# Optimization experiments

Measured on AMD Instinct MI355X. Metric: run time of the kernel, lower is better.

## Reference

```python
import jax, jax.numpy as jnp
import numpy as np

N_HEAD = 16


def setup_inputs() -> dict:
    key = jax.random.key(0)
    k1, k2, k3 = jax.random.split(key, 3)
    B, T, C = 2, 2048, 1024
    x = jax.random.normal(k1, (B, T, C), dtype=jnp.float32)
    # Linear params (torch Linear: y = x @ W.T + b), scaled for stability
    w_attn = jax.random.normal(k2, (3 * C, C), dtype=jnp.float32) * (C ** -0.5)
    b_attn = jnp.zeros((3 * C,), dtype=jnp.float32)
    w_proj = jax.random.normal(k3, (C, C), dtype=jnp.float32) * (C ** -0.5)
    b_proj = jnp.zeros((C,), dtype=jnp.float32)
    return {"x": x, "w_attn": w_attn, "b_attn": b_attn,
            "w_proj": w_proj, "b_proj": b_proj}


def reference(x, w_attn, b_attn, w_proj, b_proj):
    B, T, C = x.shape
    H = N_HEAD
    hd = C // H
    # qkv projection: [B, T, 3C]
    qkv = jnp.einsum('btc,dc->btd', x, w_attn) + b_attn
    # NOTE: original views as (B, T, H, 3*hd) then splits last dim -> per-head
    # interleaved qkv layout (NOT the standard 3-way split of full projection).
    qkv = qkv.reshape(B, T, H, 3 * hd).transpose(0, 2, 1, 3)  # [B, H, T, 3*hd]
    q, k, v = qkv[..., :hd], qkv[..., hd:2 * hd], qkv[..., 2 * hd:]
    # NOTE: scale uses full embedding dim C, not head_dim (faithful to source).
    attn = jnp.einsum('bhqd,bhkd->bhqk', q, k) * (C ** -0.5)
    # NOTE: no causal mask in the original despite the class name.
    attn = jax.nn.softmax(attn, axis=-1)
    y = jnp.einsum('bhqk,bhkd->bhqd', attn, v)  # [B, H, T, hd]
    y = y.transpose(0, 2, 1, 3).reshape(B, T, C)
    y = jnp.einsum('btc,dc->btd', y, w_proj) + b_proj
    return y
```

## Files before the change

kernel.cpp:

```cpp
#include <hip/hip_runtime.h>
#include <hip/hip_bf16.h>

typedef unsigned short u16;
typedef __bf16 bf16x8 __attribute__((ext_vector_type(8)));
typedef float f32x4 __attribute__((ext_vector_type(4)));
typedef float f32x16 __attribute__((ext_vector_type(16)));
typedef unsigned u32x4 __attribute__((ext_vector_type(4)));

#define QSCALE 0.045084220027780106f

__device__ __forceinline__ u16 f2b(float f) {
  unsigned x = __float_as_uint(f);
  unsigned r = (x + 0x7fffu + ((x >> 16) & 1u)) >> 16;
  return (u16)r;
}

__device__ __forceinline__ void gll16(const void* g, void* l) {
  __builtin_amdgcn_global_load_lds((const __attribute__((address_space(1))) void*)g,
                                   (__attribute__((address_space(3))) void*)l, 16, 0, 0);
}

__device__ __forceinline__ f32x4 mfma16(bf16x8 a, bf16x8 b, f32x4 c) {
  return __builtin_amdgcn_mfma_f32_16x16x32_bf16(a, b, c, 0, 0, 0);
}
__device__ __forceinline__ f32x16 mfma32(bf16x8 a, bf16x8 b, f32x16 c) {
  return __builtin_amdgcn_mfma_f32_32x32x16_bf16(a, b, c, 0, 0, 0);
}

__device__ __forceinline__ void plswap(unsigned& a, unsigned& b) {
  asm volatile("v_permlane32_swap_b32 %0, %1" : "+v"(a), "+v"(b));
}
__device__ __forceinline__ unsigned cvtpk(float lo, float hi) {
  unsigned r;
  asm("v_cvt_pk_bf16_f32 %0, %1, %2" : "=v"(r) : "v"(lo), "v"(hi));
  return r;
}

#if __has_builtin(__builtin_amdgcn_exp2f)
__device__ __forceinline__ float fexp2(float x) { return __builtin_amdgcn_exp2f(x); }
#else
__device__ __forceinline__ float fexp2(float x) {
  float r;
  asm("v_exp_f32 %0, %1" : "=v"(r) : "v"(x));
  return r;
}
#endif

#define WAITV(N) asm volatile("s_waitcnt vmcnt(" #N ")" ::: "memory")
#define BAR()                              \
  do {                                     \
    __builtin_amdgcn_s_barrier();          \
    __builtin_amdgcn_sched_barrier(0);     \
  } while (0)

__global__ __launch_bounds__(256) void cvt3(const float* __restrict__ x,
                                            const float* __restrict__ wa,
                                            const float* __restrict__ wp,
                                            u16* __restrict__ dx,
                                            u16* __restrict__ dwa,
                                            u16* __restrict__ dwp) {
  const int N1 = 4194304, N2 = 3145728;
  int i = (blockIdx.x * 256 + threadIdx.x) * 4;
  const float* s;
  u16* d;
  int off;
  if (i < N1) { s = x; d = dx; off = i; }
  else if (i < N1 + N2) { s = wa; d = dwa; off = i - N1; }
  else { s = wp; d = dwp; off = i - N1 - N2; }
  float4 v = *(const float4*)(s + off);
  ushort4 o;
  o.x = f2b(v.x); o.y = f2b(v.y); o.z = f2b(v.z); o.w = f2b(v.w);
  *(ushort4*)(d + off) = o;
}

__global__ __launch_bounds__(256) void gemm_qkv(const u16* __restrict__ A,
                                                const u16* __restrict__ W,
                                                const float* __restrict__ bias,
                                                u16* __restrict__ Qb,
                                                u16* __restrict__ Kb,
                                                u16* __restrict__ Vtb) {
  __shared__ u16 As[2][128 * 64];
  __shared__ u16 Bs[2][192 * 64];
  const int K = 1024;
  int o = blockIdx.x;
  int xcd = o & 7, li = o >> 3;
  int bm = (xcd >> 1) * 8 + (li >> 3);
  int bn = (xcd & 1) * 8 + (li & 7);
  int tid = threadIdx.x, lane = tid & 63, w = tid >> 6;
  int wm = w >> 1, wn = w & 1, g = lane >> 4, c = lane & 15;
  f32x4 acc[4][6] = {};
  const u16* Arow = A + (size_t)(bm * 128) * K;
  const u16* Wrow = W + (size_t)(bn * 192) * K;

  const u16* asrc[4];
  const u16* bsrc[6];
  int adst[4], bdst[6];
#pragma unroll
  for (int rr = 0; rr < 4; ++rr) {
    int ci = rr * 256 + tid;
    int row = ci >> 3, sseg = (ci & 7) ^ (row & 7);
    asrc[rr] = Arow + (size_t)row * K + sseg * 8;
    adst[rr] = ci * 8;
  }
#pragma unroll
  for (int rr = 0; rr < 6; ++rr) {
    int ci = rr * 256 + tid;
    int row = ci >> 3, sseg = (ci & 7) ^ (row & 7);
    bsrc[rr] = Wrow + (size_t)row * K + sseg * 8;
    bdst[rr] = ci * 8;
  }
  auto stage = [&](int buf) {
#pragma unroll
    for (int rr = 0; rr < 4; ++rr) gll16(asrc[rr], &As[buf][adst[rr]]);
#pragma unroll
    for (int rr = 0; rr < 6; ++rr) gll16(bsrc[rr], &Bs[buf][bdst[rr]]);
#pragma unroll
    for (int rr = 0; rr < 4; ++rr) asrc[rr] += 64;
#pragma unroll
    for (int rr = 0; rr < 6; ++rr) bsrc[rr] += 64;
  };

  stage(0);
  for (int t = 0; t < 16; ++t) {
    int cur = t & 1;
    if (t < 15) {
      stage(cur ^ 1);
      WAITV(10);
    } else {
      WAITV(0);
    }
    BAR();
#pragma unroll
    for (int kk = 0; kk < 2; ++kk) {
      int q = kk * 4 + g;
      bf16x8 af[4], bfr[6];
#pragma unroll
      for (int mi = 0; mi < 4; ++mi) {
        int row = wm * 64 + mi * 16 + c;
        af[mi] = *(const bf16x8*)&As[cur][row * 64 + ((q ^ (row & 7)) * 8)];
      }
#pragma unroll
      for (int ni = 0; ni < 6; ++ni) {
        int row = wn * 96 + ni * 16 + c;
        bfr[ni] = *(const bf16x8*)&Bs[cur][row * 64 + ((q ^ (row & 7)) * 8)];
      }
      __builtin_amdgcn_s_setprio(1);
#pragma unroll
      for (int mi = 0; mi < 4; ++mi)
#pragma unroll
        for (int ni = 0; ni < 6; ++ni)
          acc[mi][ni] = mfma16(af[mi], bfr[ni], acc[mi][ni]);
      __builtin_amdgcn_s_setprio(0);
    }
    BAR();
  }

  __syncthreads();
  u16* VT = &As[0][0];
  int b = bm >> 4;
  int tbase = (bm & 15) << 7;
  int bh = b * 16 + bn;

  int cls[6], qkoff[6], vb[6], vx[6];
  float bi[6];
#pragma unroll
  for (int ni = 0; ni < 6; ++ni) {
    int j = wn * 96 + ni * 16 + c;
    bi[ni] = bias[bn * 192 + j];
    if (j < 64) { cls[ni] = 0; qkoff[ni] = bh * 131072 + j; }
    else if (j < 128) { cls[ni] = 1; qkoff[ni] = bh * 131072 + (j - 64); }
    else { cls[ni] = 2; int vcl = j - 128; vb[ni] = vcl * 128; vx[ni] = (vcl & 15) << 3; }
  }
#pragma unroll
  for (int mi = 0; mi < 4; ++mi)
#pragma unroll
    for (int r = 0; r < 4; ++r) {
      int trow = wm * 64 + mi * 16 + g * 4 + r;
      int t = tbase + trow;
#pragma unroll
      for (int ni = 0; ni < 6; ++ni) {
        float v = acc[mi][ni][r] + bi[ni];
        if (cls[ni] == 0) Qb[(size_t)qkoff[ni] + t * 64] = f2b(v * QSCALE);
        else if (cls[ni] == 1) Kb[(size_t)qkoff[ni] + t * 64] = f2b(v);
        else VT[vb[ni] + (trow ^ vx[ni])] = f2b(v);
      }
    }
  __syncthreads();
  for (int id = tid; id < 64 * 16; id += 256) {
    int vcl = id >> 4, tc = id & 15;
    bf16x8 vv = *(const bf16x8*)&VT[vcl * 128 + ((tc * 8) ^ ((vcl & 15) << 3))];
    size_t dst = ((size_t)bh * 64 + vcl) * 2048 + tbase + tc * 8;
    *(bf16x8*)&Vtb[dst] = vv;
  }
}

__global__ __launch_bounds__(256, 4) void attn_kernel(const u16* __restrict__ Qb,
                                                      const u16* __restrict__ Kb,
                                                      const u16* __restrict__ Vtb,
                                                      u16* __restrict__ Yb) {
  __shared__ u16 SMEM[2][2][2][2048];
  int bh = blockIdx.y;
  int b = bh >> 4, hh = bh & 15;
  int tid = threadIdx.x, lane = tid & 63, wv = tid >> 6;
  int wq = wv & 1, wk = wv >> 1;
  int c5 = lane & 31, h = lane >> 5;
  int q0 = blockIdx.x * 64 + wq * 32;
  const u16* Qh = Qb + (size_t)bh * 2048 * 64;
  const u16* Kh = Kb + (size_t)bh * 2048 * 64;
  const u16* Vh = Vtb + (size_t)bh * 64 * 2048;

  const u16* Qrow = Qh + (size_t)(q0 + c5) * 64;
  bf16x8 qf[4];
#pragma unroll
  for (int dc = 0; dc < 4; ++dc)
    qf[dc] = *(const bf16x8*)&Qrow[dc * 16 + h * 8];

  f32x16 acc0 = {}, acc1 = {};
  float ls = 0.f;

  const u16* gsrc[4];
  int gstep[4];
  u16* ld0[4];
  u16* ld1[4];
#pragma unroll
  for (int part = 0; part < 4; ++part) {
    int ci = part * 256 + tid;
    int st = ci >> 9;
    int rem = ci & 511;
    int kv = rem >> 8;
    int slot = rem & 255;
    int row = slot >> 3, seg = slot & 7;
    int sseg = seg ^ (row & 7);
    int t0 = st * 1024;
    if (kv == 0) {
      gsrc[part] = Kh + (size_t)(t0 + row) * 64 + sseg * 8;
      gstep[part] = 32 * 64;
    } else {
      int dh = sseg >> 2, ksl = sseg & 3;
      gsrc[part] = Vh + (size_t)(dh * 32 + row) * 2048 + t0 + ksl * 8;
      gstep[part] = 32;
    }
    ld0[part] = &SMEM[st][0][kv][slot * 8];
    ld1[part] = &SMEM[st][1][kv][slot * 8];
  }
  auto stagepair = [&](int buf) {
#pragma unroll
    for (int part = 0; part < 4; ++part) {
      gll16(gsrc[part], buf ? ld1[part] : ld0[part]);
      gsrc[part] += gstep[part];
    }
  };

  auto tilecompute = [&](int cur) {
    const u16* Kt = &SMEM[wk][cur][0][0];
    const u16* Vt = &SMEM[wk][cur][1][0];

    f32x16 s0 = {};
    __builtin_amdgcn_s_setprio(1);
#pragma unroll
    for (int dc = 0; dc < 4; ++dc) {
      bf16x8 kf = *(const bf16x8*)&Kt[c5 * 64 + (((dc * 2 + h) ^ (c5 & 7)) * 8)];
      s0 = mfma32(kf, qf[dc], s0);
    }
    __builtin_amdgcn_s_setprio(0);

#pragma unroll
    for (int j = 0; j < 16; ++j) s0[j] = fexp2(s0[j]);
    float t4[4];
#pragma unroll
    for (int i = 0; i < 4; ++i)
      t4[i] = (s0[i] + s0[i + 4]) + (s0[i + 8] + s0[i + 12]);
    ls += (t4[0] + t4[1]) + (t4[2] + t4[3]);

    unsigned w0[8];
#pragma unroll
    for (int q2 = 0; q2 < 4; ++q2)
#pragma unroll
      for (int pp = 0; pp < 2; ++pp)
        w0[q2 * 2 + pp] = cvtpk(s0[q2 * 4 + 2 * pp], s0[q2 * 4 + 2 * pp + 1]);

    __builtin_amdgcn_s_setprio(1);
#pragma unroll
    for (int ks2 = 0; ks2 < 2; ++ks2) {
      unsigned a0 = w0[4 * ks2 + 0], b0 = w0[4 * ks2 + 2];
      unsigned a1 = w0[4 * ks2 + 1], b1 = w0[4 * ks2 + 3];
      plswap(a0, b0);
      plswap(a1, b1);
      u32x4 aw = {a0, a1, b0, b1};
      bf16x8 af = __builtin_bit_cast(bf16x8, aw);
      bf16x8 vf0 = *(const bf16x8*)&Vt[c5 * 64 + (((ks2 * 2 + h) ^ (c5 & 7)) * 8)];
      bf16x8 vf1 = *(const bf16x8*)&Vt[c5 * 64 + (((4 + ks2 * 2 + h) ^ (c5 & 7)) * 8)];
      acc0 = mfma32(af, vf0, acc0);
      acc1 = mfma32(af, vf1, acc1);
    }
    __builtin_amdgcn_s_setprio(0);
  };

  stagepair(0);
  for (int it2 = 0; it2 < 16; ++it2) {
    stagepair(1);
    WAITV(4);
    BAR();
    tilecompute(0);
    BAR();
    if (it2 < 15) {
      stagepair(0);
      WAITV(4);
    } else {
      WAITV(0);
    }
    BAR();
    tilecompute(1);
    BAR();
  }

  float* MG = (float*)&SMEM[0][0][0][0];
  int gi = wq * 64 + lane;
  __syncthreads();
  if (wk == 1) {
    MG[gi] = ls;
#pragma unroll
    for (int j = 0; j < 16; ++j) {
      MG[128 + gi * 33 + j] = acc0[j];
      MG[128 + gi * 33 + 16 + j] = acc1[j];
    }
  }
  __syncthreads();
  if (wk == 0) {
    float l2 = ls + MG[gi];
    l2 += __shfl_xor(l2, 32);
    float inv = 1.0f / l2;
#pragma unroll
    for (int j = 0; j < 16; ++j) {
      int q = (j & 3) + 8 * (j >> 2) + 4 * h;
      float ibq = __shfl(inv, q, 64);
      float y0 = (acc0[j] + MG[128 + gi * 33 + j]) * ibq;
      float y1 = (acc1[j] + MG[128 + gi * 33 + 16 + j]) * ibq;
      int trow = q0 + q;
      size_t base = ((size_t)b * 2048 + trow) * 1024 + hh * 64;
      Yb[base + c5] = f2b(y0);
      Yb[base + 32 + c5] = f2b(y1);
    }
  }
}

__global__ __launch_bounds__(512) void gemm_proj(const u16* __restrict__ A,
                                                 const u16* __restrict__ W,
                                                 const float* __restrict__ bias,
                                                 float* __restrict__ out) {
  __shared__ u16 As[4][128 * 64];
  __shared__ u16 Bs[4][128 * 64];
  const int K = 1024;
  int o = blockIdx.x;
  int bn = o & 7, bm = o >> 3;
  int tid = threadIdx.x, lane = tid & 63, w = tid >> 6;
  int wm = w >> 1, wn = w & 1, g = lane >> 4, c = lane & 15;
  f32x4 acc[2][4] = {};
  const u16* Arow = A + (size_t)(bm * 128) * K;
  const u16* Wrow = W + (size_t)(bn * 128) * K;

  const u16* asrc[2];
  const u16* bsrc[2];
  int sdst[2];
#pragma unroll
  for (int rr = 0; rr < 2; ++rr) {
    int ci = rr * 512 + tid;
    int row = ci >> 3, sseg = (ci & 7) ^ (row & 7);
    asrc[rr] = Arow + (size_t)row * K + sseg * 8;
    bsrc[rr] = Wrow + (size_t)row * K + sseg * 8;
    sdst[rr] = ci * 8;
  }
  auto stage = [&](int step) {
    int slot = step & 3;
#pragma unroll
    for (int rr = 0; rr < 2; ++rr) gll16(asrc[rr], &As[slot][sdst[rr]]);
#pragma unroll
    for (int rr = 0; rr < 2; ++rr) gll16(bsrc[rr], &Bs[slot][sdst[rr]]);
#pragma unroll
    for (int rr = 0; rr < 2; ++rr) { asrc[rr] += 64; bsrc[rr] += 64; }
  };

  auto compute = [&](int step) {
    int slot = step & 3;
#pragma unroll
    for (int kk = 0; kk < 2; ++kk) {
      int q = kk * 4 + g;
      bf16x8 af[2], bfr[4];
#pragma unroll
      for (int mi = 0; mi < 2; ++mi) {
        int row = wm * 32 + mi * 16 + c;
        af[mi] = *(const bf16x8*)&As[slot][row * 64 + ((q ^ (row & 7)) * 8)];
      }
#pragma unroll
      for (int ni = 0; ni < 4; ++ni) {
        int row = wn * 64 + ni * 16 + c;
        bfr[ni] = *(const bf16x8*)&Bs[slot][row * 64 + ((q ^ (row & 7)) * 8)];
      }
#pragma unroll
      for (int mi = 0; mi < 2; ++mi)
#pragma unroll
        for (int ni = 0; ni < 4; ++ni)
          acc[mi][ni] = mfma16(af[mi], bfr[ni], acc[mi][ni]);
    }
  };

  stage(0);
  stage(1);
  stage(2);
  for (int t = 0; t <= 13; ++t) {
    WAITV(8);
    BAR();
    if (t <= 12) stage(t + 3);
    compute(t);
  }
  WAITV(4);
  BAR();
  compute(14);
  WAITV(0);
  BAR();
  compute(15);

#pragma unroll
  for (int mi = 0; mi < 2; ++mi)
#pragma unroll
    for (int ni = 0; ni < 4; ++ni)
#pragma unroll
      for (int r = 0; r < 4; ++r) {
        int row = bm * 128 + wm * 32 + mi * 16 + g * 4 + r;
        int col = bn * 128 + wn * 64 + ni * 16 + c;
        out[(size_t)row * 1024 + col] = acc[mi][ni][r] + bias[col];
      }
}

extern "C" void kernel_launch(void* const* d_in, const int* in_sizes, int n_in,
                              void* d_out, int out_size, void* d_ws, size_t ws_size,
                              hipStream_t stream) {
  const float* x      = (const float*)d_in[0];
  const float* w_attn = (const float*)d_in[1];
  const float* b_attn = (const float*)d_in[2];
  const float* w_proj = (const float*)d_in[3];
  const float* b_proj = (const float*)d_in[4];
  float* out = (float*)d_out;

  u16* ws = (u16*)d_ws;
  const size_t XB  = 0;
  const size_t WAB = XB + 4194304;
  const size_t WPB = WAB + 3145728;
  const size_t QB  = WPB + 1048576;
  const size_t KB  = QB + 4194304;
  const size_t VTB = KB + 4194304;
  const size_t YB  = VTB + 4194304;

  cvt3<<<8192, 256, 0, stream>>>(x, w_attn, w_proj, ws + XB, ws + WAB, ws + WPB);

  gemm_qkv<<<512, 256, 0, stream>>>(ws + XB, ws + WAB, b_attn,
                                    ws + QB, ws + KB, ws + VTB);

  attn_kernel<<<dim3(32, 32), 256, 0, stream>>>(ws + QB, ws + KB, ws + VTB, ws + YB);

  gemm_proj<<<256, 512, 0, stream>>>(ws + YB, ws + WPB, b_proj, out);
}
```

Measured before the change: 110.5 us.

## Fuse fp32-to-bf16 conversion of x into the QKV GEMM A-tile loads

```diff
diff --git a/kernel.cpp b/kernel.cpp
--- a/kernel.cpp
+++ b/kernel.cpp
@@ -47,33 +47,31 @@
 #endif
 
 #define WAITV(N) asm volatile("s_waitcnt vmcnt(" #N ")" ::: "memory")
+#define WAITLGKM0() asm volatile("s_waitcnt lgkmcnt(0)" ::: "memory")
 #define BAR()                              \
   do {                                     \
     __builtin_amdgcn_s_barrier();          \
     __builtin_amdgcn_sched_barrier(0);     \
   } while (0)
 
-__global__ __launch_bounds__(256) void cvt3(const float* __restrict__ x,
-                                            const float* __restrict__ wa,
+__global__ __launch_bounds__(256) void cvt2(const float* __restrict__ wa,
                                             const float* __restrict__ wp,
-                                            u16* __restrict__ dx,
                                             u16* __restrict__ dwa,
                                             u16* __restrict__ dwp) {
-  const int N1 = 4194304, N2 = 3145728;
+  const int N2 = 3145728;
   int i = (blockIdx.x * 256 + threadIdx.x) * 4;
   const float* s;
   u16* d;
   int off;
-  if (i < N1) { s = x; d = dx; off = i; }
-  else if (i < N1 + N2) { s = wa; d = dwa; off = i - N1; }
-  else { s = wp; d = dwp; off = i - N1 - N2; }
+  if (i < N2) { s = wa; d = dwa; off = i; }
+  else { s = wp; d = dwp; off = i - N2; }
   float4 v = *(const float4*)(s + off);
   ushort4 o;
   o.x = f2b(v.x); o.y = f2b(v.y); o.z = f2b(v.z); o.w = f2b(v.w);
   *(ushort4*)(d + off) = o;
 }
 
-__global__ __launch_bounds__(256) void gemm_qkv(const u16* __restrict__ A,
+__global__ __launch_bounds__(256) void gemm_qkv(const float* __restrict__ A32,
                                                 const u16* __restrict__ W,
                                                 const float* __restrict__ bias,
                                                 u16* __restrict__ Qb,
@@ -89,19 +87,19 @@
   int tid = threadIdx.x, lane = tid & 63, w = tid >> 6;
   int wm = w >> 1, wn = w & 1, g = lane >> 4, c = lane & 15;
   f32x4 acc[4][6] = {};
-  const u16* Arow = A + (size_t)(bm * 128) * K;
   const u16* Wrow = W + (size_t)(bn * 192) * K;
 
-  const u16* asrc[4];
+  const float* a32src[4];
+  int awdst[4];
+#pragma unroll
+  for (int p = 0; p < 4; ++p) {
+    int ci = p * 256 + tid;
+    int row = ci >> 3, seg = ci & 7;
+    a32src[p] = A32 + (size_t)(bm * 128 + row) * K + seg * 8;
+    awdst[p] = row * 64 + ((seg ^ (row & 7)) * 8);
+  }
   const u16* bsrc[6];
-  int adst[4], bdst[6];
-#pragma unroll
-  for (int rr = 0; rr < 4; ++rr) {
-    int ci = rr * 256 + tid;
-    int row = ci >> 3, sseg = (ci & 7) ^ (row & 7);
-    asrc[rr] = Arow + (size_t)row * K + sseg * 8;
-    adst[rr] = ci * 8;
-  }
+  int bdst[6];
 #pragma unroll
   for (int rr = 0; rr < 6; ++rr) {
     int ci = rr * 256 + tid;
@@ -109,27 +107,35 @@
     bsrc[rr] = Wrow + (size_t)row * K + sseg * 8;
     bdst[rr] = ci * 8;
   }
-  auto stage = [&](int buf) {
-#pragma unroll
-    for (int rr = 0; rr < 4; ++rr) gll16(asrc[rr], &As[buf][adst[rr]]);
-#pragma unroll
-    for (int rr = 0; rr < 6; ++rr) gll16(bsrc[rr], &Bs[buf][bdst[rr]]);
-#pragma unroll
-    for (int rr = 0; rr < 4; ++rr) asrc[rr] += 64;
-#pragma unroll
-    for (int rr = 0; rr < 6; ++rr) bsrc[rr] += 64;
+
+  float4 rA0[8], rA1[8];
+#define ISSUE_A(RA)                                        \
+  do {                                                     \
+    _Pragma("unroll") for (int p = 0; p < 4; ++p) {        \
+      RA[2 * p] = *(const float4*)(a32src[p]);             \
+      RA[2 * p + 1] = *(const float4*)(a32src[p] + 4);     \
+      a32src[p] += 64;                                     \
+    }                                                      \
+  } while (0)
+#define WRITE_A(buf, RA)                                   \
+  do {                                                     \
+    _Pragma("unroll") for (int p = 0; p < 4; ++p) {        \
+      u32x4 wv = {cvtpk(RA[2 * p].x, RA[2 * p].y),         \
+                  cvtpk(RA[2 * p].z, RA[2 * p].w),         \
+                  cvtpk(RA[2 * p + 1].x, RA[2 * p + 1].y), \
+                  cvtpk(RA[2 * p + 1].z, RA[2 * p + 1].w)};\
+      *(u32x4*)&As[buf][awdst[p]] = wv;                    \
+    }                                                      \
+  } while (0)
+
+  auto issueB = [&](int buf) {
+#pragma unroll
+    for (int rr = 0; rr < 6; ++rr) {
+      gll16(bsrc[rr], &Bs[buf][bdst[rr]]);
+      bsrc[rr] += 64;
+    }
   };
-
-  stage(0);
-  for (int t = 0; t < 16; ++t) {
-    int cur = t & 1;
-    if (t < 15) {
-      stage(cur ^ 1);
-      WAITV(10);
-    } else {
-      WAITV(0);
-    }
-    BAR();
+  auto compute = [&](int buf) {
 #pragma unroll
     for (int kk = 0; kk < 2; ++kk) {
       int q = kk * 4 + g;
@@ -137,12 +143,12 @@
 #pragma unroll
       for (int mi = 0; mi < 4; ++mi) {
         int row = wm * 64 + mi * 16 + c;
-        af[mi] = *(const bf16x8*)&As[cur][row * 64 + ((q ^ (row & 7)) * 8)];
+        af[mi] = *(const bf16x8*)&As[buf][row * 64 + ((q ^ (row & 7)) * 8)];
       }
 #pragma unroll
       for (int ni = 0; ni < 6; ++ni) {
         int row = wn * 96 + ni * 16 + c;
-        bfr[ni] = *(const bf16x8*)&Bs[cur][row * 64 + ((q ^ (row & 7)) * 8)];
+        bfr[ni] = *(const bf16x8*)&Bs[buf][row * 64 + ((q ^ (row & 7)) * 8)];
       }
       __builtin_amdgcn_s_setprio(1);
 #pragma unroll
@@ -152,8 +158,45 @@
           acc[mi][ni] = mfma16(af[mi], bfr[ni], acc[mi][ni]);
       __builtin_amdgcn_s_setprio(0);
     }
-    BAR();
-  }
+  };
+
+  ISSUE_A(rA0);
+  issueB(0);
+  ISSUE_A(rA1);
+  issueB(1);
+  WAITV(14);
+  WRITE_A(0, rA0);
+  WAITLGKM0();
+  BAR();
+
+  for (int it = 0; it < 8; ++it) {
+    if (it < 7) ISSUE_A(rA0);
+    compute(0);
+    BAR();
+    if (it < 7) issueB(0);
+    if (it < 7) {
+      WAITV(14);
+    } else {
+      WAITV(0);
+    }
+    WRITE_A(1, rA1);
+    WAITLGKM0();
+    BAR();
+    if (it < 7) {
+      ISSUE_A(rA1);
+      compute(1);
+      BAR();
+      issueB(1);
+      WAITV(14);
+      WRITE_A(0, rA0);
+      WAITLGKM0();
+      BAR();
+    } else {
+      compute(1);
+    }
+  }
+#undef ISSUE_A
+#undef WRITE_A
 
   __syncthreads();
   u16* VT = &As[0][0];
@@ -443,17 +486,16 @@
   float* out = (float*)d_out;
 
   u16* ws = (u16*)d_ws;
-  const size_t XB  = 0;
-  const size_t WAB = XB + 4194304;
+  const size_t WAB = 4194304;
   const size_t WPB = WAB + 3145728;
   const size_t QB  = WPB + 1048576;
   const size_t KB  = QB + 4194304;
   const size_t VTB = KB + 4194304;
   const size_t YB  = VTB + 4194304;
 
-  cvt3<<<8192, 256, 0, stream>>>(x, w_attn, w_proj, ws + XB, ws + WAB, ws + WPB);
-
-  gemm_qkv<<<512, 256, 0, stream>>>(ws + XB, ws + WAB, b_attn,
+  cvt2<<<4096, 256, 0, stream>>>(w_attn, w_proj, ws + WAB, ws + WPB);
+
+  gemm_qkv<<<512, 256, 0, stream>>>(x, ws + WAB, b_attn,
                                     ws + QB, ws + KB, ws + VTB);
 
   attn_kernel<<<dim3(32, 32), 256, 0, stream>>>(ws + QB, ws + KB, ws + VTB, ws + YB);
```

After: 135.4 us. 1.23x slower.
